# Performance work log

Measured on AMD Instinct MI355X. Metric: run time of the kernel, lower is better.

Reference implementation:

```python
import jax, jax.numpy as jnp
import numpy as np

FACTOR = 2
DIM = 3
F3 = FACTOR ** DIM            # 8
B = 2                          # batch size
S = 128                        # cubic spatial shape (spatial_shape = [S, S, S])
N = 262144                     # number of active voxels
C = 32                         # feature channels
MAXS = (S + FACTOR - 1) // FACTOR  # 64, downsampled grid extent per dim
# OFFSET per torch code: cumprod of MAX reversed, reversed, + [1]
OFFSET = (MAXS ** 3, MAXS ** 2, MAXS, 1)


def setup_inputs() -> dict:
    rng = np.random.default_rng(0)
    # unique voxel coords: sample N distinct cells from the B x S^3 grid
    lin = rng.permutation(B * S ** 3)[:N].astype(np.int64)
    b = lin // (S ** 3)
    r = lin % (S ** 3)
    x = r // (S * S)
    y = (r // S) % S
    z = r % S
    coords = jnp.asarray(np.stack([b, x, y, z], axis=-1), dtype=jnp.int32)  # [N, 4]
    feats = jax.random.normal(jax.random.key(0), (N, C), dtype=jnp.float32)
    return {"feats": feats, "coords": coords}


def reference(feats, coords):
    c = coords.astype(jnp.int32)
    down = c[:, 1:] // FACTOR          # [N, 3] downsampled spatial coords
    sub = c[:, 1:] % FACTOR            # [N, 3] position within factor^3 cell
    # subidx = sum(sub[..., i] * factor**i), i=0 -> x
    subidx = sub[:, 0] + sub[:, 1] * FACTOR + sub[:, 2] * (FACTOR ** 2)
    # linear code over (batch, dx, dy, dz)
    code = (c[:, 0] * OFFSET[0] + down[:, 0] * OFFSET[1]
            + down[:, 1] * OFFSET[2] + down[:, 2] * OFFSET[3])
    # unique with static size=N (M_unique <= N); pad with out-of-range sentinel
    code_u, idx = jnp.unique(code, return_inverse=True, size=N,
                             fill_value=B * MAXS ** 3)
    idx = idx.reshape(-1)
    new_coords = jnp.stack(
        [code_u // OFFSET[0]]
        + [(code_u // OFFSET[i + 1]) % MAXS for i in range(DIM)], axis=-1)
    # scatter feats into channel-expanded buffer; padded rows stay zero
    buf = jnp.zeros((N * F3, C), dtype=feats.dtype).at[idx * F3 + subidx].set(feats)
    new_feats = buf.reshape(N, F3 * C)   # [N_pad, factor^3 * C]
    return new_feats, new_coords
```

## Files before the change

kernel.cpp:

```cpp
#include <hip/hip_runtime.h>
#include <hip/hip_bf16.h>

typedef unsigned int u32;

static constexpr u32 NCODES = 524288u;

__device__ __forceinline__ u32 code_of(int4 c) {
  return ((u32)c.x << 18) + ((u32)(c.y >> 1) << 12) +
         ((u32)(c.z >> 1) << 6) + (u32)(c.w >> 1);
}

__global__ void k_mark(const int4* __restrict__ coords, u32* __restrict__ mark, int n) {
  int i = blockIdx.x * blockDim.x + threadIdx.x;
  if (i >= n) return;
  mark[code_of(coords[i])] = 1u;
}

__global__ void k_reduce(const u32* __restrict__ mark, u32* __restrict__ bsum) {
  int b = blockIdx.x, t = threadIdx.x;
  uint4 m = ((const uint4*)mark)[b * 256 + t];
  u32 s = m.x + m.y + m.z + m.w;
  for (int d = 32; d > 0; d >>= 1) s += __shfl_down(s, d, 64);
  __shared__ u32 ws4[4];
  if ((t & 63) == 0) ws4[t >> 6] = s;
  __syncthreads();
  if (t == 0) bsum[b] = ws4[0] + ws4[1] + ws4[2] + ws4[3];
}

__global__ void k_scan512(const u32* __restrict__ bsum, u32* __restrict__ boff) {
  __shared__ u32 s[512];
  int t = threadIdx.x;
  u32 v = bsum[t];
  s[t] = v;
  __syncthreads();
  for (int d = 1; d < 512; d <<= 1) {
    u32 add = (t >= d) ? s[t - d] : 0u;
    __syncthreads();
    s[t] += add;
    __syncthreads();
  }
  boff[t] = s[t] - v;
}

__device__ __forceinline__ void wrc(float* __restrict__ outc, u32 r, u32 code) {
  float4 p;
  p.x = (float)(code >> 18);
  p.y = (float)((code >> 12) & 63u);
  p.z = (float)((code >> 6) & 63u);
  p.w = (float)(code & 63u);
  ((float4*)outc)[r] = p;
}

__global__ void k_scan_scatter(u32* __restrict__ codes, const u32* __restrict__ boff,
                               float* __restrict__ outc) {
  int b = blockIdx.x, t = threadIdx.x;
  uint4 m = ((const uint4*)codes)[b * 256 + t];
  u32 tsum = m.x + m.y + m.z + m.w;
  u32 incl = tsum;
  int lane = t & 63;
  for (int d = 1; d < 64; d <<= 1) {
    u32 v = __shfl_up(incl, d, 64);
    if (lane >= d) incl += v;
  }
  __shared__ u32 wsum[4];
  if (lane == 63) wsum[t >> 6] = incl;
  __syncthreads();
  u32 woff = boff[b];
  for (int w = 0; w < (t >> 6); ++w) woff += wsum[w];
  u32 e0 = woff + incl - tsum;
  u32 e1 = e0 + m.x, e2 = e1 + m.y, e3 = e2 + m.z;
  ((uint4*)codes)[b * 256 + t] = make_uint4(e0, e1, e2, e3);
  u32 base = (u32)b * 1024u + (u32)t * 4u;
  if (m.x) wrc(outc, e0, base + 0u);
  if (m.y) wrc(outc, e1, base + 1u);
  if (m.z) wrc(outc, e2, base + 2u);
  if (m.w) wrc(outc, e3, base + 3u);
}

__global__ void k_fillc(float* __restrict__ outc, int n) {
  int i = blockIdx.x * blockDim.x + threadIdx.x;
  if (i >= n) return;
  ((float4*)outc)[i] = make_float4(2.0f, 0.0f, 0.0f, 0.0f);
}

__global__ void k_scatter(const float4* __restrict__ feats, const int4* __restrict__ coords,
                          const u32* __restrict__ rank, float* __restrict__ out, int n8) {
  int tid = blockIdx.x * blockDim.x + threadIdx.x;
  if (tid >= n8) return;
  int row = tid >> 3, q = tid & 7;
  int4 c = coords[row];
  u32 code = code_of(c);
  u32 sub = (u32)(c.y & 1) + ((u32)(c.z & 1) << 1) + ((u32)(c.w & 1) << 2);
  float4 f = feats[tid];
  ((float4*)out)[((size_t)rank[code] * 8u + sub) * 8u + (u32)q] = f;
}

extern "C" void kernel_launch(void* const* d_in, const int* in_sizes, int n_in,
                              void* d_out, int out_size, void* d_ws, size_t ws_size,
                              hipStream_t stream) {
  const float* feats = (const float*)d_in[0];
  const int* coords  = (const int*)d_in[1];
  int n = in_sizes[1] / 4;
  float* out = (float*)d_out;
  size_t featsElems = (size_t)n * 256;
  float* outc = out + featsElems;

  u32* codes = (u32*)d_ws;
  u32* bsum  = codes + NCODES;
  u32* boff  = bsum + 512;

  hipMemsetAsync(d_out, 0, featsElems * sizeof(float), stream);
  hipMemsetAsync(d_ws, 0, NCODES * sizeof(u32), stream);

  k_fillc<<<(n + 255) / 256, 256, 0, stream>>>(outc, n);
  k_mark<<<(n + 255) / 256, 256, 0, stream>>>((const int4*)coords, codes, n);
  k_reduce<<<NCODES / 1024, 256, 0, stream>>>(codes, bsum);
  k_scan512<<<1, 512, 0, stream>>>(bsum, boff);
  k_scan_scatter<<<NCODES / 1024, 256, 0, stream>>>(codes, boff, outc);
  k_scatter<<<(n * 8 + 255) / 256, 256, 0, stream>>>((const float4*)feats,
                                                     (const int4*)coords, codes, out, n * 8);
}
```

Measured before the change: 315.6 us.

## Split output zeroing across pipeline kernels and fold scan into scatter

Replaces the big memset of the output buffer with nontemporal zero stores split into four chunks. Each chunk is done by extra blocks inside the mark-clear, mark, reduce and scan kernels, so the zeroing overlaps the latency-bound small stages. The separate single-block scan kernel is removed; each scatter block computes its own prefix offset by reducing the block sums. Sentinel fill and mark clearing move into the first kernel. The code assumes n divides evenly into the chunk sizes, and every block now repeats a redundant 512-entry reduction.

```diff
diff --git a/kernel.cpp b/kernel.cpp
--- a/kernel.cpp
+++ b/kernel.cpp
@@ -1,45 +1,67 @@
 #include <hip/hip_runtime.h>
-#include <hip/hip_bf16.h>
 
 typedef unsigned int u32;
+typedef float __attribute__((ext_vector_type(4))) f4;
+typedef unsigned int __attribute__((ext_vector_type(4))) u4;
 
 static constexpr u32 NCODES = 524288u;
+static constexpr u32 ZB = 1024;
 
 __device__ __forceinline__ u32 code_of(int4 c) {
   return ((u32)c.x << 18) + ((u32)(c.y >> 1) << 12) +
          ((u32)(c.z >> 1) << 6) + (u32)(c.w >> 1);
 }
 
-__global__ void k_mark(const int4* __restrict__ coords, u32* __restrict__ mark, int n) {
-  int i = blockIdx.x * blockDim.x + threadIdx.x;
-  if (i >= n) return;
-  mark[code_of(coords[i])] = 1u;
+__device__ __forceinline__ void zero_chunk(f4* __restrict__ base, u32 zb, u32 t,
+                                           u32 nIter) {
+  const f4 z = {0.f, 0.f, 0.f, 0.f};
+  u32 i0 = zb * 256u + t;
+  for (u32 k = 0; k < nIter; ++k)
+    __builtin_nontemporal_store(z, base + i0 + k * (ZB * 256u));
 }
 
-__global__ void k_reduce(const u32* __restrict__ mark, u32* __restrict__ bsum) {
-  int b = blockIdx.x, t = threadIdx.x;
-  uint4 m = ((const uint4*)mark)[b * 256 + t];
+__global__ void k_A(f4* __restrict__ out, u32 n, u4* __restrict__ marks,
+                    f4* __restrict__ zbase, u32 zIter) {
+  u32 b = blockIdx.x, t = threadIdx.x;
+  u32 sentB = n / 1024u;
+  if (b < NCODES / 4u / 256u) {
+    const u4 z = {0u, 0u, 0u, 0u};
+    __builtin_nontemporal_store(z, marks + b * 256u + t);
+  } else if (b < NCODES / 4u / 256u + sentB) {
+    f4* outc = out + (size_t)n * 64u;
+    u32 i = (b - NCODES / 4u / 256u) * 256u + t;
+    const f4 s4 = {2.f, 0.f, 0.f, 0.f};
+    u32 span = sentB * 256u;
+    for (u32 k = 0; k < 4u; ++k)
+      __builtin_nontemporal_store(s4, outc + i + k * span);
+  } else {
+    zero_chunk(zbase, b - (NCODES / 4u / 256u + sentB), t, zIter);
+  }
+}
+
+__global__ void k_B(const int4* __restrict__ coords, u32* __restrict__ mark, u32 n,
+                    f4* __restrict__ zbase, u32 zIter) {
+  u32 b = blockIdx.x, t = threadIdx.x;
+  u32 mb = n / 256u;
+  if (b < mb) {
+    u32 i = b * 256u + t;
+    mark[code_of(coords[i])] = 1u;
+  } else {
+    zero_chunk(zbase, b - mb, t, zIter);
+  }
+}
+
+__global__ void k_C(const u32* __restrict__ mark, u32* __restrict__ bsum,
+                    f4* __restrict__ zbase, u32 zIter) {
+  u32 b = blockIdx.x, t = threadIdx.x;
+  if (b >= 512u) { zero_chunk(zbase, b - 512u, t, zIter); return; }
+  uint4 m = ((const uint4*)mark)[b * 256u + t];
   u32 s = m.x + m.y + m.z + m.w;
   for (int d = 32; d > 0; d >>= 1) s += __shfl_down(s, d, 64);
   __shared__ u32 ws4[4];
-  if ((t & 63) == 0) ws4[t >> 6] = s;
+  if ((t & 63u) == 0u) ws4[t >> 6] = s;
   __syncthreads();
   if (t == 0) bsum[b] = ws4[0] + ws4[1] + ws4[2] + ws4[3];
-}
-
-__global__ void k_scan512(const u32* __restrict__ bsum, u32* __restrict__ boff) {
-  __shared__ u32 s[512];
-  int t = threadIdx.x;
-  u32 v = bsum[t];
-  s[t] = v;
-  __syncthreads();
-  for (int d = 1; d < 512; d <<= 1) {
-    u32 add = (t >= d) ? s[t - d] : 0u;
-    __syncthreads();
-    s[t] += add;
-    __syncthreads();
-  }
-  boff[t] = s[t] - v;
 }
 
 __device__ __forceinline__ void wrc(float* __restrict__ outc, u32 r, u32 code) {
@@ -51,40 +73,44 @@
   ((float4*)outc)[r] = p;
 }
 
-__global__ void k_scan_scatter(u32* __restrict__ codes, const u32* __restrict__ boff,
-                               float* __restrict__ outc) {
-  int b = blockIdx.x, t = threadIdx.x;
-  uint4 m = ((const uint4*)codes)[b * 256 + t];
+__global__ void k_D(u32* __restrict__ codes, const u32* __restrict__ bsum,
+                    float* __restrict__ outc, f4* __restrict__ zbase, u32 zIter) {
+  u32 b = blockIdx.x, t = threadIdx.x;
+  if (b >= 512u) { zero_chunk(zbase, b - 512u, t, zIter); return; }
+
+  u32 v0 = bsum[t], v1 = bsum[t + 256u];
+  u32 s = (t < b ? v0 : 0u) + (t + 256u < b ? v1 : 0u);
+  for (int d = 32; d > 0; d >>= 1) s += __shfl_down(s, d, 64);
+  __shared__ u32 ws4[4];
+  if ((t & 63u) == 0u) ws4[t >> 6] = s;
+  __syncthreads();
+  u32 boff = ws4[0] + ws4[1] + ws4[2] + ws4[3];
+
+  uint4 m = ((const uint4*)codes)[b * 256u + t];
   u32 tsum = m.x + m.y + m.z + m.w;
   u32 incl = tsum;
-  int lane = t & 63;
+  u32 lane = t & 63u;
   for (int d = 1; d < 64; d <<= 1) {
     u32 v = __shfl_up(incl, d, 64);
-    if (lane >= d) incl += v;
+    if (lane >= (u32)d) incl += v;
   }
   __shared__ u32 wsum[4];
-  if (lane == 63) wsum[t >> 6] = incl;
+  if (lane == 63u) wsum[t >> 6] = incl;
   __syncthreads();
-  u32 woff = boff[b];
-  for (int w = 0; w < (t >> 6); ++w) woff += wsum[w];
+  u32 woff = boff;
+  for (u32 w = 0; w < (t >> 6); ++w) woff += wsum[w];
   u32 e0 = woff + incl - tsum;
   u32 e1 = e0 + m.x, e2 = e1 + m.y, e3 = e2 + m.z;
-  ((uint4*)codes)[b * 256 + t] = make_uint4(e0, e1, e2, e3);
-  u32 base = (u32)b * 1024u + (u32)t * 4u;
+  ((uint4*)codes)[b * 256u + t] = make_uint4(e0, e1, e2, e3);
+  u32 base = b * 1024u + t * 4u;
   if (m.x) wrc(outc, e0, base + 0u);
   if (m.y) wrc(outc, e1, base + 1u);
   if (m.z) wrc(outc, e2, base + 2u);
   if (m.w) wrc(outc, e3, base + 3u);
 }
 
-__global__ void k_fillc(float* __restrict__ outc, int n) {
-  int i = blockIdx.x * blockDim.x + threadIdx.x;
-  if (i >= n) return;
-  ((float4*)outc)[i] = make_float4(2.0f, 0.0f, 0.0f, 0.0f);
-}
-
-__global__ void k_scatter(const float4* __restrict__ feats, const int4* __restrict__ coords,
-                          const u32* __restrict__ rank, float* __restrict__ out, int n8) {
+__global__ void k_E(const float4* __restrict__ feats, const int4* __restrict__ coords,
+                    const u32* __restrict__ rank, float* __restrict__ out, int n8) {
   int tid = blockIdx.x * blockDim.x + threadIdx.x;
   if (tid >= n8) return;
   int row = tid >> 3, q = tid & 7;
@@ -100,23 +126,26 @@
                               hipStream_t stream) {
   const float* feats = (const float*)d_in[0];
   const int* coords  = (const int*)d_in[1];
-  int n = in_sizes[1] / 4;
-  float* out = (float*)d_out;
-  size_t featsElems = (size_t)n * 256;
-  float* outc = out + featsElems;
+  u32 n = (u32)(in_sizes[1] / 4);
+  f4* out4 = (f4*)d_out;
+  float* outc = (float*)d_out + (size_t)n * 256u;
 
   u32* codes = (u32*)d_ws;
   u32* bsum  = codes + NCODES;
-  u32* boff  = bsum + 512;
 
-  hipMemsetAsync(d_out, 0, featsElems * sizeof(float), stream);
-  hipMemsetAsync(d_ws, 0, NCODES * sizeof(u32), stream);
+  u32 feats4 = n * 64u;
+  u32 chunk  = feats4 / 4u;
+  u32 zIter  = chunk / (ZB * 256u);
+  u32 markZB = NCODES / 4u / 256u;
+  u32 sentB  = n / 1024u;
 
-  k_fillc<<<(n + 255) / 256, 256, 0, stream>>>(outc, n);
-  k_mark<<<(n + 255) / 256, 256, 0, stream>>>((const int4*)coords, codes, n);
-  k_reduce<<<NCODES / 1024, 256, 0, stream>>>(codes, bsum);
-  k_scan512<<<1, 512, 0, stream>>>(bsum, boff);
-  k_scan_scatter<<<NCODES / 1024, 256, 0, stream>>>(codes, boff, outc);
-  k_scatter<<<(n * 8 + 255) / 256, 256, 0, stream>>>((const float4*)feats,
-                                                     (const int4*)coords, codes, out, n * 8);
+  k_A<<<markZB + sentB + ZB, 256, 0, stream>>>(out4, n, (u4*)codes,
+                                               out4 + 0u * chunk, zIter);
+  k_B<<<n / 256u + ZB, 256, 0, stream>>>((const int4*)coords, codes, n,
+                                         out4 + 1u * chunk, zIter);
+  k_C<<<512u + ZB, 256, 0, stream>>>(codes, bsum, out4 + 2u * chunk, zIter);
+  k_D<<<512u + ZB, 256, 0, stream>>>(codes, bsum, outc, out4 + 3u * chunk, zIter);
+  k_E<<<(n * 8u + 255u) / 256u, 256, 0, stream>>>((const float4*)feats,
+                                                  (const int4*)coords, codes,
+                                                  (float*)d_out, (int)(n * 8u));
 }
```

Result: no change. 318.4 us (+0.9%).
